# Kernel tuning notes

Measured on AMD Instinct MI355X. Metric: run time of the kernel, lower is better.

The kernel has to match this reference:

```python
import jax, jax.numpy as jnp
import numpy as np

APREC = 8   # activation fractional bits
PPREC = 8   # parameter fractional bits
IWIDTH = 3  # integer width -> clamp to [-2**IWIDTH, 2**IWIDTH - 1]

QMAX = 2.0 ** IWIDTH - 1.0
QMIN = -(2.0 ** IWIDTH)


def quant(v, prec):
    # round to 2**-prec grid (torch.round and jnp.round both round-half-to-even)
    s = 2.0 ** prec
    return jnp.round(v * s) / s


def round_max(v):
    # the relu-chain in the source is exactly a clamp to [QMIN, QMAX]
    return jnp.clip(v, QMIN, QMAX)


def fixed_point_conv(x, w, b):
    """Quantized 'conv': each elementwise product w[j,m,p,q]*x[b,m,k+p,l+q] is
    rounded to the activation grid and clamped BEFORE summation, then bias added.
    x: [B,Cin,H,W], w: [Cout,Cin,K,K], b: [Cout].
    Loop is over the KxK fixed kernel offsets (25), fully vectorized over B/Cout/Cin/space."""
    w = quant(w, PPREC)
    b = quant(b, PPREC)
    K = w.shape[2]
    Ho = x.shape[2] - K + 1
    Wo = x.shape[3] - K + 1
    out = jnp.zeros((x.shape[0], w.shape[0], Ho, Wo), dtype=x.dtype)
    for p in range(K):
        for q in range(K):
            # [B, Cout, Cin, Ho, Wo]
            prod = x[:, None, :, p:p + Ho, q:q + Wo] * w[None, :, :, p, q, None, None]
            prod = round_max(quant(prod, APREC))
            out = out + prod.sum(axis=2)
    return out + b[None, :, None, None]


def fixed_point_fc(x, w, b):
    # x: [B, in], w: [out, in], b: [out]
    w = round_max(quant(w, PPREC))
    b = round_max(quant(b, PPREC))
    x = round_max(quant(x, APREC))
    out = x @ w.T + b[None, :]
    out = round_max(out)
    return quant(out, APREC)


def max_pool2(x):
    return jax.lax.reduce_window(x, -jnp.inf, jax.lax.max,
                                 (1, 1, 2, 2), (1, 1, 2, 2), 'VALID')


def setup_inputs() -> dict:
    key = jax.random.key(0)
    ks = jax.random.split(key, 9)
    B = 2048
    return {
        'x': jax.random.normal(ks[0], (B, 1, 28, 28), jnp.float32),
        'conv1_w': jax.random.normal(ks[1], (10, 1, 5, 5), jnp.float32) * 0.2,
        'conv1_b': jax.random.normal(ks[2], (10,), jnp.float32) * 0.1,
        'conv2_w': jax.random.normal(ks[3], (20, 10, 5, 5), jnp.float32) * 0.1,
        'conv2_b': jax.random.normal(ks[4], (20,), jnp.float32) * 0.1,
        'fc1_w': jax.random.normal(ks[5], (50, 320), jnp.float32) * 0.05,
        'fc1_b': jax.random.normal(ks[6], (50,), jnp.float32) * 0.05,
        'fc2_w': jax.random.normal(ks[7], (10, 50), jnp.float32) * 0.1,
        'fc2_b': jax.random.normal(ks[8], (10,), jnp.float32) * 0.1,
    }


def reference(x, conv1_w, conv1_b, conv2_w, conv2_b, fc1_w, fc1_b, fc2_w, fc2_b):
    x = quant(x, APREC)
    conv1_input = x
    x = fixed_point_conv(x, conv1_w, conv1_b)          # [B,10,24,24]
    x = quant(x, APREC)
    conv1_output = x
    x = jax.nn.relu(max_pool2(x))                      # [B,10,12,12]
    x = quant(x, APREC)
    conv2_input = x
    x = fixed_point_conv(x, conv2_w, conv2_b)          # [B,20,8,8]
    x = quant(x, APREC)
    conv2_output = x
    # Dropout2d / F.dropout are identity in eval mode
    x = jax.nn.relu(max_pool2(x))                      # [B,20,4,4]
    x = x.reshape(-1, 320)
    x = quant(x, APREC)
    fc1_input = x
    x = fixed_point_fc(x, fc1_w, fc1_b)                # [B,50]
    x = quant(x, APREC)
    fc1_output = x
    x = jax.nn.relu(x)
    x = quant(x, APREC)
    fc2_input = x
    x = fixed_point_fc(x, fc2_w, fc2_b)                # [B,10]
    x = quant(x, APREC)
    fc2_output = x
    logp = jax.nn.log_softmax(x, axis=1)
    return (logp, conv1_input, conv1_output, conv2_input, conv2_output,
            fc1_input, fc1_output, fc2_input, fc2_output)
```

## Files before the change

kernel.cpp:

```cpp
#include <hip/hip_runtime.h>
#include <math.h>


#define NB 2048

#define OFF_LOGP   0
#define OFF_C1IN   (OFF_LOGP  + NB*10)
#define OFF_C1OUT  (OFF_C1IN  + NB*784)
#define OFF_C2IN   (OFF_C1OUT + NB*5760)
#define OFF_C2OUT  (OFF_C2IN  + NB*1440)
#define OFF_FC1IN  (OFF_C2OUT + NB*1280)
#define OFF_FC1OUT (OFF_FC1IN + NB*320)
#define OFF_FC2IN  (OFF_FC1OUT+ NB*50)
#define OFF_FC2OUT (OFF_FC2IN + NB*50)

#define MAGIC_F 12582912.0f

#define WS_WT1 0
#define WS_B1  20480
#define WS_WT2 20544
#define WS_B2  21344
#define WS_CW2 21360
#define WS_CB2 26960
#define WS_CW1 26980
#define WS_CB1 27260

__device__ __forceinline__ float clamp8(float v) {
    return __builtin_amdgcn_fmed3f(v, -8.0f, 7.0f);
}

__global__ __launch_bounds__(256)
void k0_prep(const float* __restrict__ cw1, const float* __restrict__ cb1,
             const float* __restrict__ cw2, const float* __restrict__ cb2,
             const float* __restrict__ fw1, const float* __restrict__ fb1,
             const float* __restrict__ fw2, const float* __restrict__ fb2,
             float* __restrict__ ws)
{
    const int t = threadIdx.x, b = blockIdx.x;
    if (b < 50) {
        const float* src = fw1 + b * 320;
        for (int i = t; i < 320; i += 256)
            ws[WS_WT1 + i * 64 + b] = clamp8(rintf(src[i] * 256.0f) * (1.0f / 256.0f));
    } else if (b == 50) {
        for (int idx = t; idx < 320 * 14; idx += 256) {
            int i = idx / 14, j = 50 + idx % 14;
            ws[WS_WT1 + i * 64 + j] = 0.0f;
        }
        for (int idx = t; idx < 800; idx += 256) {
            int k = idx >> 4, j = idx & 15;
            ws[WS_WT2 + idx] = (j < 10) ? clamp8(rintf(fw2[j * 50 + k] * 256.0f) * (1.0f / 256.0f)) : 0.0f;
        }
        if (t < 64) ws[WS_B1 + t] = (t < 50) ? clamp8(rintf(fb1[t] * 256.0f) * (1.0f / 256.0f)) : 0.0f;
        if (t < 16) ws[WS_B2 + t] = (t < 10) ? clamp8(rintf(fb2[t] * 256.0f) * (1.0f / 256.0f)) : 0.0f;
    } else {
        for (int idx = t; idx < 5600; idx += 256) {
            int cc = idx / 28, col = idx % 28;
            ws[WS_CW2 + idx] = (col < 25) ? rintf(cw2[cc * 25 + col] * 256.0f) : 0.0f;
        }
        if (t < 20) ws[WS_CB2 + t] = rintf(cb2[t] * 256.0f);
        for (int idx = t; idx < 280; idx += 256) {
            int cc = idx / 28, col = idx % 28;
            ws[WS_CW1 + idx] = (col < 25) ? rintf(cw1[cc * 25 + col] * 256.0f) : 0.0f;
        }
        if (t >= 32 && t < 42) ws[WS_CB1 + (t - 32)] = rintf(cb1[t - 32] * 256.0f);
    }
}

__global__ __launch_bounds__(256, 8)
void k12w(const float* __restrict__ x, const float* __restrict__ ws,
          float* __restrict__ out)
{
    __shared__ __align__(16) float s_x[784];
    __shared__ __align__(16) float s_p1[1440];

    const int t   = threadIdx.x;
    const int img = blockIdx.x;
    const int wv  = t >> 6;
    const int L   = t & 63;

    {
        const float* xg = x + (size_t)img * 784;
        float* c1in_g = out + OFF_C1IN + (size_t)img * 784;
        for (int i = t; i < 784; i += 256) {
            float v = rintf(xg[i] * 256.0f) * (1.0f / 256.0f);
            s_x[i] = v;
            c1in_g[i] = v;
        }
    }
    __syncthreads();

    if (L < 60) {
        const int c5 = L / 12;
        const int r  = L % 12;
        const int ii = r >> 1;
        const int jh = r & 1;
        const int i  = wv * 6 + ii;

        for (int h = 0; h < 2; h++) {
            asm volatile("" ::: "memory");
            const int co = h * 5 + c5;
            float wreg[28];
            {
                const float* wb = ws + WS_CW1 + co * 28;
                #pragma unroll
                for (int k = 0; k < 7; k++) {
                    float4 v4 = *(const float4*)(wb + 4 * k);
                    wreg[4*k] = v4.x; wreg[4*k+1] = v4.y; wreg[4*k+2] = v4.z; wreg[4*k+3] = v4.w;
                }
            }
            float acc[12];
            #pragma unroll
            for (int j = 0; j < 12; j++) acc[j] = MAGIC_F;
            #pragma unroll
            for (int p = 0; p < 5; p++) {
                float xr[16];
                const float* row = s_x + (i + p) * 28 + 12 * jh;
                #pragma unroll
                for (int k = 0; k < 4; k++) {
                    float4 v4 = *(const float4*)(row + 4 * k);
                    xr[4*k] = v4.x; xr[4*k+1] = v4.y; xr[4*k+2] = v4.z; xr[4*k+3] = v4.w;
                }
                #pragma unroll
                for (int q = 0; q < 5; q++) {
                    float w = wreg[p * 5 + q];
                    #pragma unroll
                    for (int j = 0; j < 12; j++)
                        acc[j] = fmaf(xr[q + j], w, acc[j]);
                }
            }
            const float C = MAGIC_F - ws[WS_CB1 + co];
            float v[12];
            #pragma unroll
            for (int j = 0; j < 12; j++) v[j] = (acc[j] - C) * (1.0f / 256.0f);

            float* gdst = out + OFF_C1OUT + (size_t)img * 5760 + co * 576 + i * 24 + 12 * jh;
            #pragma unroll
            for (int k = 0; k < 3; k++) {
                float4 st = { v[4*k], v[4*k+1], v[4*k+2], v[4*k+3] };
                *(float4*)(gdst + 4 * k) = st;
            }

            float m[6];
            #pragma unroll
            for (int j2 = 0; j2 < 6; j2++) m[j2] = fmaxf(v[2*j2], v[2*j2+1]);
            float pm[6];
            #pragma unroll
            for (int j2 = 0; j2 < 6; j2++) pm[j2] = __shfl_xor(m[j2], 2);

            if ((ii & 1) == 0) {
                float pr[6];
                #pragma unroll
                for (int j2 = 0; j2 < 6; j2++)
                    pr[j2] = fmaxf(fmaxf(m[j2], pm[j2]), 0.0f);
                const int o = co * 144 + (i >> 1) * 12 + 6 * jh;
                float* g = out + OFF_C2IN + (size_t)img * 1440 + o;
                #pragma unroll
                for (int k = 0; k < 3; k++) {
                    float2 st = { pr[2*k], pr[2*k+1] };
                    *(float2*)(g + 2 * k) = st;
                    *(float2*)(s_p1 + o + 2 * k) = st;
                }
            }
        }
    }
    __syncthreads();

    const int ch = t & 1;
    const int i2 = (t >> 1) & 7;

    auto conv2_body = [&](int co) {
        float acc[8];
        #pragma unroll
        for (int j = 0; j < 8; j++) acc[j] = MAGIC_F;

        #pragma unroll
        for (int cc = 0; cc < 5; cc++) {
            const int ci = ch * 5 + cc;
            float wreg[28];
            {
                const float* wb = ws + WS_CW2 + (co * 10 + ci) * 28;
                #pragma unroll
                for (int k = 0; k < 7; k++) {
                    float4 v4 = *(const float4*)(wb + 4 * k);
                    wreg[4*k] = v4.x; wreg[4*k+1] = v4.y; wreg[4*k+2] = v4.z; wreg[4*k+3] = v4.w;
                }
            }
            const float* xb = s_p1 + ci * 144;
            #pragma unroll
            for (int p = 0; p < 5; p++) {
                const float* row = xb + (i2 + p) * 12;
                float4 a4 = *(const float4*)(row);
                float4 b4 = *(const float4*)(row + 4);
                float4 c4 = *(const float4*)(row + 8);
                float xr[12] = { a4.x, a4.y, a4.z, a4.w, b4.x, b4.y, b4.z, b4.w,
                                 c4.x, c4.y, c4.z, c4.w };
                #pragma unroll
                for (int q = 0; q < 5; q++) {
                    float w = wreg[p * 5 + q];
                    #pragma unroll
                    for (int j = 0; j < 8; j++)
                        acc[j] = fmaf(xr[q + j], w, acc[j]);
                }
            }
        }

        float s[8];
        #pragma unroll
        for (int j = 0; j < 8; j++) s[j] = acc[j] - MAGIC_F;
        #pragma unroll
        for (int j = 0; j < 8; j++) s[j] += __shfl_xor(s[j], 1);

        const float b2 = ws[WS_CB2 + co];
        float v[8];
        #pragma unroll
        for (int j = 0; j < 8; j++) v[j] = (s[j] + b2) * (1.0f / 256.0f);

        float m[4], pm[4];
        #pragma unroll
        for (int c = 0; c < 4; c++) m[c] = fmaxf(v[2*c], v[2*c+1]);
        #pragma unroll
        for (int c = 0; c < 4; c++) pm[c] = __shfl_xor(m[c], 2);

        if (ch == 0) {
            float4 st0 = { v[0], v[1], v[2], v[3] };
            float4 st1 = { v[4], v[5], v[6], v[7] };
            float* cdst = out + OFF_C2OUT + (size_t)img * 1280 + co * 64 + i2 * 8;
            *(float4*)(cdst)     = st0;
            *(float4*)(cdst + 4) = st1;

            if ((i2 & 1) == 0) {
                float4 pr = { fmaxf(fmaxf(m[0], pm[0]), 0.0f),
                              fmaxf(fmaxf(m[1], pm[1]), 0.0f),
                              fmaxf(fmaxf(m[2], pm[2]), 0.0f),
                              fmaxf(fmaxf(m[3], pm[3]), 0.0f) };
                const int o = co * 16 + (i2 >> 1) * 4;
                *(float4*)(out + OFF_FC1IN + (size_t)img * 320 + o) = pr;
                float4 prc = { clamp8(pr.x), clamp8(pr.y), clamp8(pr.z), clamp8(pr.w) };
                *(float4*)(s_x + o) = prc;
            }
        }
    };

    for (int co0 = t >> 4; co0 < 20; co0 += 16) {
        asm volatile("" ::: "memory");
        conv2_body(co0);
    }
    __syncthreads();

    if (wv == 0) {
        const float* sf = s_x;
        float acc = ws[WS_B1 + L];
        #pragma unroll 8
        for (int k = 0; k < 320; k++)
            acc = fmaf(sf[k], ws[WS_WT1 + k * 64 + L], acc);
        float o1 = rintf(clamp8(acc) * 256.0f) * (1.0f / 256.0f);
        float r1 = fmaxf(o1, 0.0f);
        if (L < 50) {
            out[OFF_FC1OUT + (size_t)img * 50 + L] = o1;
            out[OFF_FC2IN  + (size_t)img * 50 + L] = r1;
        }
        float yc = clamp8(r1);

        float acc2 = ws[WS_B2 + (L & 15)];
        #pragma unroll 10
        for (int k = 0; k < 50; k++) {
            float yk = __shfl(yc, k);
            acc2 = fmaf(yk, ws[WS_WT2 + k * 16 + (L & 15)], acc2);
        }
        float o2 = rintf(clamp8(acc2) * 256.0f) * (1.0f / 256.0f);
        if (L < 10) out[OFF_FC2OUT + (size_t)img * 10 + L] = o2;

        float vmx = (L < 10) ? o2 : -3.0e38f;
        #pragma unroll
        for (int d = 1; d < 16; d <<= 1)
            vmx = fmaxf(vmx, __shfl_xor(vmx, d, 16));
        float e = (L < 10) ? expf(o2 - vmx) : 0.0f;
        #pragma unroll
        for (int d = 1; d < 16; d <<= 1)
            e += __shfl_xor(e, d, 16);
        float lse = vmx + logf(e);
        if (L < 10) out[OFF_LOGP + (size_t)img * 10 + L] = o2 - lse;
    }
}

extern "C" void kernel_launch(void* const* d_in, const int* in_sizes, int n_in,
                              void* d_out, int out_size, void* d_ws, size_t ws_size,
                              hipStream_t stream) {
    const float* x   = (const float*)d_in[0];
    const float* cw1 = (const float*)d_in[1];
    const float* cb1 = (const float*)d_in[2];
    const float* cw2 = (const float*)d_in[3];
    const float* cb2 = (const float*)d_in[4];
    const float* fw1 = (const float*)d_in[5];
    const float* fb1 = (const float*)d_in[6];
    const float* fw2 = (const float*)d_in[7];
    const float* fb2 = (const float*)d_in[8];
    float* o  = (float*)d_out;
    float* ws = (float*)d_ws;

    k0_prep<<<52, 256, 0, stream>>>(cw1, cb1, cw2, cb2, fw1, fb1, fw2, fb2, ws);
    k12w   <<<NB, 256, 0, stream>>>(x, ws, o);
}
```

Baseline: 153.4 us.

## Compute two output channels per thread in conv1 and conv2 to reuse inputs

Conv1 now computes both output-channel halves at once in each thread, reusing every loaded input row for two weight sets. Conv2 is restructured so 160 threads each handle two output channels (g and g+10), sharing the shared-memory input loads across both, instead of 256 threads looping over channels with some idle on the second pass. This doubles register use, so launch bounds drop from 8 to 4 blocks per CU. Fewer concurrent blocks and the unroll-1 loops may reduce latency hiding, and 96 threads now sit idle during conv2.

Result: slower. 174.0 us (+13.4%).

```diff
diff --git a/kernel.cpp b/kernel.cpp
--- a/kernel.cpp
+++ b/kernel.cpp
@@ -66,7 +66,7 @@
     }
 }
 
-__global__ __launch_bounds__(256, 8)
+__global__ __launch_bounds__(256, 4)
 void k12w(const float* __restrict__ x, const float* __restrict__ ws,
           float* __restrict__ out)
 {
@@ -96,38 +96,45 @@
         const int jh = r & 1;
         const int i  = wv * 6 + ii;
 
-        for (int h = 0; h < 2; h++) {
-            asm volatile("" ::: "memory");
-            const int co = h * 5 + c5;
-            float wreg[28];
-            {
-                const float* wb = ws + WS_CW1 + co * 28;
-                #pragma unroll
-                for (int k = 0; k < 7; k++) {
-                    float4 v4 = *(const float4*)(wb + 4 * k);
-                    wreg[4*k] = v4.x; wreg[4*k+1] = v4.y; wreg[4*k+2] = v4.z; wreg[4*k+3] = v4.w;
-                }
-            }
-            float acc[12];
-            #pragma unroll
-            for (int j = 0; j < 12; j++) acc[j] = MAGIC_F;
-            #pragma unroll
-            for (int p = 0; p < 5; p++) {
-                float xr[16];
-                const float* row = s_x + (i + p) * 28 + 12 * jh;
-                #pragma unroll
-                for (int k = 0; k < 4; k++) {
-                    float4 v4 = *(const float4*)(row + 4 * k);
-                    xr[4*k] = v4.x; xr[4*k+1] = v4.y; xr[4*k+2] = v4.z; xr[4*k+3] = v4.w;
-                }
-                #pragma unroll
-                for (int q = 0; q < 5; q++) {
-                    float w = wreg[p * 5 + q];
-                    #pragma unroll
-                    for (int j = 0; j < 12; j++)
-                        acc[j] = fmaf(xr[q + j], w, acc[j]);
-                }
-            }
+        float wregA[28], wregB[28];
+        {
+            const float* wa = ws + WS_CW1 + c5 * 28;
+            const float* wb = ws + WS_CW1 + (c5 + 5) * 28;
+            #pragma unroll
+            for (int k = 0; k < 7; k++) {
+                float4 a4 = *(const float4*)(wa + 4 * k);
+                float4 b4 = *(const float4*)(wb + 4 * k);
+                wregA[4*k]=a4.x; wregA[4*k+1]=a4.y; wregA[4*k+2]=a4.z; wregA[4*k+3]=a4.w;
+                wregB[4*k]=b4.x; wregB[4*k+1]=b4.y; wregB[4*k+2]=b4.z; wregB[4*k+3]=b4.w;
+            }
+        }
+
+        float accA[12], accB[12];
+        #pragma unroll
+        for (int j = 0; j < 12; j++) { accA[j] = MAGIC_F; accB[j] = MAGIC_F; }
+
+        #pragma unroll 1
+        for (int p = 0; p < 5; p++) {
+            float xr[16];
+            const float* row = s_x + (i + p) * 28 + 12 * jh;
+            #pragma unroll
+            for (int k = 0; k < 4; k++) {
+                float4 v4 = *(const float4*)(row + 4 * k);
+                xr[4*k] = v4.x; xr[4*k+1] = v4.y; xr[4*k+2] = v4.z; xr[4*k+3] = v4.w;
+            }
+            #pragma unroll
+            for (int q = 0; q < 5; q++) {
+                const float wA = wregA[p * 5 + q];
+                const float wB = wregB[p * 5 + q];
+                #pragma unroll
+                for (int j = 0; j < 12; j++) {
+                    accA[j] = fmaf(xr[q + j], wA, accA[j]);
+                    accB[j] = fmaf(xr[q + j], wB, accB[j]);
+                }
+            }
+        }
+
+        auto epiA = [&](int co, float* acc) {
             const float C = MAGIC_F - ws[WS_CB1 + co];
             float v[12];
             #pragma unroll
@@ -161,28 +168,36 @@
                     *(float2*)(s_p1 + o + 2 * k) = st;
                 }
             }
-        }
+        };
+        epiA(c5, accA);
+        epiA(c5 + 5, accB);
     }
     __syncthreads();
 
-    const int ch = t & 1;
-    const int i2 = (t >> 1) & 7;
-
-    auto conv2_body = [&](int co) {
-        float acc[8];
+    if ((t >> 4) < 10) {
+        const int g  = t >> 4;
+        const int ch = t & 1;
+        const int i2 = (t >> 1) & 7;
+
+        float accA[8], accB[8];
         #pragma unroll
-        for (int j = 0; j < 8; j++) acc[j] = MAGIC_F;
-
-        #pragma unroll
+        for (int j = 0; j < 8; j++) { accA[j] = MAGIC_F; accB[j] = MAGIC_F; }
+
+        #pragma unroll 1
         for (int cc = 0; cc < 5; cc++) {
+            asm volatile("" ::: "memory");
             const int ci = ch * 5 + cc;
-            float wreg[28];
+
+            float wregA[28], wregB[28];
             {
-                const float* wb = ws + WS_CW2 + (co * 10 + ci) * 28;
+                const float* wa = ws + WS_CW2 + (g * 10 + ci) * 28;
+                const float* wb = ws + WS_CW2 + ((g + 10) * 10 + ci) * 28;
                 #pragma unroll
                 for (int k = 0; k < 7; k++) {
-                    float4 v4 = *(const float4*)(wb + 4 * k);
-                    wreg[4*k] = v4.x; wreg[4*k+1] = v4.y; wreg[4*k+2] = v4.z; wreg[4*k+3] = v4.w;
+                    float4 a4 = *(const float4*)(wa + 4 * k);
+                    float4 b4 = *(const float4*)(wb + 4 * k);
+                    wregA[4*k]=a4.x; wregA[4*k+1]=a4.y; wregA[4*k+2]=a4.z; wregA[4*k+3]=a4.w;
+                    wregB[4*k]=b4.x; wregB[4*k+1]=b4.y; wregB[4*k+2]=b4.z; wregB[4*k+3]=b4.w;
                 }
             }
             const float* xb = s_p1 + ci * 144;
@@ -196,54 +211,56 @@
                                  c4.x, c4.y, c4.z, c4.w };
                 #pragma unroll
                 for (int q = 0; q < 5; q++) {
-                    float w = wreg[p * 5 + q];
+                    const float wA = wregA[p * 5 + q];
+                    const float wB = wregB[p * 5 + q];
                     #pragma unroll
-                    for (int j = 0; j < 8; j++)
-                        acc[j] = fmaf(xr[q + j], w, acc[j]);
-                }
-            }
-        }
-
-        float s[8];
-        #pragma unroll
-        for (int j = 0; j < 8; j++) s[j] = acc[j] - MAGIC_F;
-        #pragma unroll
-        for (int j = 0; j < 8; j++) s[j] += __shfl_xor(s[j], 1);
-
-        const float b2 = ws[WS_CB2 + co];
-        float v[8];
-        #pragma unroll
-        for (int j = 0; j < 8; j++) v[j] = (s[j] + b2) * (1.0f / 256.0f);
-
-        float m[4], pm[4];
-        #pragma unroll
-        for (int c = 0; c < 4; c++) m[c] = fmaxf(v[2*c], v[2*c+1]);
-        #pragma unroll
-        for (int c = 0; c < 4; c++) pm[c] = __shfl_xor(m[c], 2);
-
-        if (ch == 0) {
-            float4 st0 = { v[0], v[1], v[2], v[3] };
-            float4 st1 = { v[4], v[5], v[6], v[7] };
-            float* cdst = out + OFF_C2OUT + (size_t)img * 1280 + co * 64 + i2 * 8;
-            *(float4*)(cdst)     = st0;
-            *(float4*)(cdst + 4) = st1;
-
-            if ((i2 & 1) == 0) {
-                float4 pr = { fmaxf(fmaxf(m[0], pm[0]), 0.0f),
-                              fmaxf(fmaxf(m[1], pm[1]), 0.0f),
-                              fmaxf(fmaxf(m[2], pm[2]), 0.0f),
-                              fmaxf(fmaxf(m[3], pm[3]), 0.0f) };
-                const int o = co * 16 + (i2 >> 1) * 4;
-                *(float4*)(out + OFF_FC1IN + (size_t)img * 320 + o) = pr;
-                float4 prc = { clamp8(pr.x), clamp8(pr.y), clamp8(pr.z), clamp8(pr.w) };
-                *(float4*)(s_x + o) = prc;
-            }
-        }
-    };
-
-    for (int co0 = t >> 4; co0 < 20; co0 += 16) {
-        asm volatile("" ::: "memory");
-        conv2_body(co0);
+                    for (int j = 0; j < 8; j++) {
+                        accA[j] = fmaf(xr[q + j], wA, accA[j]);
+                        accB[j] = fmaf(xr[q + j], wB, accB[j]);
+                    }
+                }
+            }
+        }
+
+        auto epiB = [&](int co, float* acc) {
+            float s[8];
+            #pragma unroll
+            for (int j = 0; j < 8; j++) s[j] = acc[j] - MAGIC_F;
+            #pragma unroll
+            for (int j = 0; j < 8; j++) s[j] += __shfl_xor(s[j], 1);
+
+            const float b2 = ws[WS_CB2 + co];
+            float v[8];
+            #pragma unroll
+            for (int j = 0; j < 8; j++) v[j] = (s[j] + b2) * (1.0f / 256.0f);
+
+            float m[4], pm[4];
+            #pragma unroll
+            for (int c = 0; c < 4; c++) m[c] = fmaxf(v[2*c], v[2*c+1]);
+            #pragma unroll
+            for (int c = 0; c < 4; c++) pm[c] = __shfl_xor(m[c], 2);
+
+            if (ch == 0) {
+                float4 st0 = { v[0], v[1], v[2], v[3] };
+                float4 st1 = { v[4], v[5], v[6], v[7] };
+                float* cdst = out + OFF_C2OUT + (size_t)img * 1280 + co * 64 + i2 * 8;
+                *(float4*)(cdst)     = st0;
+                *(float4*)(cdst + 4) = st1;
+
+                if ((i2 & 1) == 0) {
+                    float4 pr = { fmaxf(fmaxf(m[0], pm[0]), 0.0f),
+                                  fmaxf(fmaxf(m[1], pm[1]), 0.0f),
+                                  fmaxf(fmaxf(m[2], pm[2]), 0.0f),
+                                  fmaxf(fmaxf(m[3], pm[3]), 0.0f) };
+                    const int o = co * 16 + (i2 >> 1) * 4;
+                    *(float4*)(out + OFF_FC1IN + (size_t)img * 320 + o) = pr;
+                    float4 prc = { clamp8(pr.x), clamp8(pr.y), clamp8(pr.z), clamp8(pr.w) };
+                    *(float4*)(s_x + o) = prc;
+                }
+            }
+        };
+        epiB(g, accA);
+        epiB(g + 10, accB);
     }
     __syncthreads();
 
```
